# Performance work log

Measured on AMD Instinct MI355X. Metric: run time of the kernel, lower is better.

## Reference

```python
import jax, jax.numpy as jnp
import numpy as np

N_NODES = 100000
N_EDGES = 1600000
DIM = 128
N_LAYERS = 3
N_GRAPHS = 2048


def setup_inputs() -> dict:
    key = jax.random.key(0)
    ks = jax.random.split(key, 6)
    x = jax.random.normal(ks[0], (N_NODES, DIM), dtype=jnp.float32)
    edge_index = jax.random.randint(ks[1], (2, N_EDGES), 0, N_NODES, dtype=jnp.int64)
    batch = jnp.sort(jax.random.randint(ks[2], (N_NODES,), 0, N_GRAPHS, dtype=jnp.int64))
    scale = 1.0 / np.sqrt(DIM)
    W1 = jax.random.normal(ks[3], (N_LAYERS, DIM, DIM), dtype=jnp.float32) * scale
    b1 = jnp.zeros((N_LAYERS, DIM), dtype=jnp.float32)
    W2 = jax.random.normal(ks[4], (N_LAYERS, DIM, DIM), dtype=jnp.float32) * scale
    b2 = jnp.zeros((N_LAYERS, DIM), dtype=jnp.float32)
    return {"x": x, "edge_index": edge_index, "batch": batch,
            "W1": W1, "b1": b1, "W2": W2, "b2": b2}


def reference(x, edge_index, batch, W1, b1, W2, b2):
    src, dst = edge_index[0], edge_index[1]
    n = x.shape[0]
    n_layers = W1.shape[0]
    for l in range(n_layers):
        # GINConv (eps=0): h_i = MLP( sum_{j in N(i)} x_j + x_i )
        agg = jax.ops.segment_sum(x[src], dst, num_segments=n)  # [N, D]
        h = agg + x
        h = jnp.maximum(h @ W1[l] + b1[l], 0.0) @ W2[l] + b2[l]
        x = jnp.maximum(h, 0.0)  # outer self.act
    # global_mean_pool over graph ids
    sums = jax.ops.segment_sum(x, batch, num_segments=N_GRAPHS)  # [G, D]
    counts = jax.ops.segment_sum(jnp.ones((n,), x.dtype), batch, num_segments=N_GRAPHS)
    return sums / jnp.maximum(counts, 1.0)[:, None]
```

## Files before the change

kernel.cpp:

```cpp
#include <hip/hip_runtime.h>
#include <hip/hip_bf16.h>
#include <stdint.h>

#define N_NODES  100000
#define N_PAD    100032
#define N_EDGES  1600000
#define DIM      128
#define N_LAYERS 3
#define N_GRAPHS 2048

#define BSHIFT   9
#define NBUCKET  196
#define P1CHUNK  8192
#define P1GRID   196

typedef _Float16 f16;
typedef __attribute__((ext_vector_type(2))) _Float16 f16x2;
typedef __attribute__((ext_vector_type(8))) _Float16 f16x8;
typedef __attribute__((ext_vector_type(4))) float f32x4;

#define MFMA16(a, b, c) __builtin_amdgcn_mfma_f32_16x16x32_f16((a), (b), (c), 0, 0, 0)

#define OFF_OFFS  0u
#define OFF_BHT   400064u
#define OFF_BST   400896u
#define OFF_GCUR  401728u
#define OFF_BLKH  402560u
#define OFF_ESRC  556288u
#define OFF_PAIR  6956288u
#define OFF_X16   19756288u
#define OFF_A16   45364480u
#define OFF_B16   70972672u
#define OFF_W1T   96580864u
#define OFF_W2T   96679168u


__global__ __launch_bounds__(256) void k_bhist(const int* __restrict__ dst,
                                               int* __restrict__ btot, int* __restrict__ blkh) {
    __shared__ int h[NBUCKET];
    int tid = threadIdx.x, b = blockIdx.x;
    if (tid < NBUCKET) h[tid] = 0;
    __syncthreads();
    int base = b * P1CHUNK;
    int n = min(P1CHUNK, N_EDGES - base);
    for (int i = tid; i < n; i += 256)
        atomicAdd(&h[dst[base + i] >> BSHIFT], 1);
    __syncthreads();
    if (tid < NBUCKET) {
        blkh[b * NBUCKET + tid] = h[tid];
        atomicAdd(&btot[tid], h[tid]);
    }
}

__global__ void k_bscan(const int* __restrict__ btot, int* __restrict__ bstart,
                        int* __restrict__ gcursor, int* __restrict__ offs) {
    __shared__ int s[NBUCKET + 1];
    if (threadIdx.x == 0) {
        int run = 0;
        for (int i = 0; i < NBUCKET; i++) { s[i] = run; run += btot[i]; }
        s[NBUCKET] = run;
    }
    __syncthreads();
    int t = threadIdx.x;
    if (t <= NBUCKET) bstart[t] = s[t];
    if (t < NBUCKET)  gcursor[t] = s[t];
    if (t == 0) offs[N_NODES] = N_EDGES;
}

__global__ __launch_bounds__(256) void k_part1(const int* __restrict__ src, const int* __restrict__ dst,
                                               const int* __restrict__ blkh, int* __restrict__ gcursor,
                                               uint2* __restrict__ pairs) {
    __shared__ int gbase[NBUCKET];
    __shared__ int cur[NBUCKET];
    int tid = threadIdx.x, b = blockIdx.x;
    if (tid < NBUCKET) {
        int h = blkh[b * NBUCKET + tid];
        gbase[tid] = atomicAdd(&gcursor[tid], h);
        cur[tid] = 0;
    }
    __syncthreads();
    int base = b * P1CHUNK;
    int n = min(P1CHUNK, N_EDGES - base);
    for (int i = tid; i < n; i += 256) {
        int d = dst[base + i], s = src[base + i];
        int bin = d >> BSHIFT;
        int slot = atomicAdd(&cur[bin], 1);
        uint2 p; p.x = (unsigned)d; p.y = (unsigned)s;
        pairs[gbase[bin] + slot] = p;
    }
}

__global__ __launch_bounds__(256) void k_part2(const uint2* __restrict__ pairs,
                                               const int* __restrict__ bstart,
                                               int* __restrict__ offs, int* __restrict__ esrc) {
    __shared__ int cnt[512];
    __shared__ int excl[512];
    __shared__ int sc[256];
    int t = threadIdx.x, b = blockIdx.x;
    int n0 = b << BSHIFT;
    int nn = min(512, N_NODES - n0);
    int e0 = bstart[b], e1 = bstart[b + 1];
    cnt[t] = 0; cnt[t + 256] = 0;
    __syncthreads();
    for (int i = e0 + t; i < e1; i += 256)
        atomicAdd(&cnt[pairs[i].x & 511], 1);
    __syncthreads();
    int a = cnt[2 * t], psum = a + cnt[2 * t + 1];
    sc[t] = psum;
    __syncthreads();
    for (int off = 1; off < 256; off <<= 1) {
        int v = (t >= off) ? sc[t - off] : 0;
        __syncthreads();
        sc[t] += v;
        __syncthreads();
    }
    int pairExcl = sc[t] - psum;
    excl[2 * t] = pairExcl;
    excl[2 * t + 1] = pairExcl + a;
    __syncthreads();
    for (int j = t; j < nn; j += 256) offs[n0 + j] = e0 + excl[j];
    __syncthreads();
    for (int i = e0 + t; i < e1; i += 256) {
        uint2 p = pairs[i];
        int pos = e0 + atomicAdd(&excl[p.x & 511], 1);
        esrc[pos] = (int)p.y;
    }
}


__global__ void k_cvtX(const float* __restrict__ x, f16* __restrict__ o) {
    size_t i = ((size_t)blockIdx.x * 256 + threadIdx.x) * 8;
    float4 v0 = *(const float4*)&x[i];
    float4 v1 = *(const float4*)&x[i + 4];
    f16x8 h;
    h[0] = (f16)v0.x; h[1] = (f16)v0.y; h[2] = (f16)v0.z; h[3] = (f16)v0.w;
    h[4] = (f16)v1.x; h[5] = (f16)v1.y; h[6] = (f16)v1.z; h[7] = (f16)v1.w;
    *(f16x8*)&o[i] = h;
}

__global__ void k_cvtW(const float* __restrict__ W, f16* __restrict__ Wt) {
    int t = blockIdx.x * 256 + threadIdx.x;
    int l = t >> 14;
    int kn = t & 16383;
    int k = kn >> 7, n = kn & 127;
    Wt[l * 16384 + n * 128 + k] = (f16)W[t];
}


__global__ __launch_bounds__(256) void k_agg(const f16* __restrict__ x, const int* __restrict__ offs,
                                             const int* __restrict__ esrc, f16* __restrict__ out) {
    int tid = threadIdx.x;
    int node = blockIdx.x * 4 + (tid >> 6);
    int lane = tid & 63;
    int g = lane >> 4;
    int c = lane & 15;
    const f16x8* xr = (const f16x8*)x;
    int e0 = offs[node], e1 = offs[node + 1];

    float acc[8];
    f16x8 sv = xr[(size_t)node * 16 + c];
#pragma unroll
    for (int j = 0; j < 8; j++) acc[j] = (g == 0) ? (float)sv[j] : 0.f;

    int e = e0 + g;
    for (; e + 4 < e1; e += 8) {
        int s0 = esrc[e], s1 = esrc[e + 4];
        f16x8 v0 = xr[(size_t)s0 * 16 + c];
        f16x8 v1 = xr[(size_t)s1 * 16 + c];
#pragma unroll
        for (int j = 0; j < 8; j++) acc[j] += (float)v0[j] + (float)v1[j];
    }
    if (e < e1) {
        f16x8 v = xr[(size_t)esrc[e] * 16 + c];
#pragma unroll
        for (int j = 0; j < 8; j++) acc[j] += (float)v[j];
    }

#pragma unroll
    for (int j = 0; j < 8; j++) {
        acc[j] += __shfl_xor(acc[j], 16);
        acc[j] += __shfl_xor(acc[j], 32);
    }
    if (g == 0) {
        f16x8 o;
#pragma unroll
        for (int j = 0; j < 8; j++) o[j] = (f16)acc[j];
        ((f16x8*)out)[(size_t)node * 16 + c] = o;
    }
}


#define BM 64
#define LDS_K 136

__global__ __launch_bounds__(256) void k_mlp(const f16* __restrict__ in, f16* __restrict__ out,
                                             const f16* __restrict__ W1t, const float* __restrict__ b1,
                                             const f16* __restrict__ W2t, const float* __restrict__ b2) {
    __shared__ __align__(16) f16 tile[BM * LDS_K];
    int tid = threadIdx.x;
    int lane = tid & 63;
    int w = tid >> 6;
    int fr = lane & 15;
    int fg = lane >> 4;
    int row0 = blockIdx.x * BM;

    f16x8 w1f[2][4], w2f[2][4];
    float b1v[2], b2v[2];
#pragma unroll
    for (int nt = 0; nt < 2; nt++) {
        int col = w * 32 + nt * 16 + fr;
#pragma unroll
        for (int ks = 0; ks < 4; ks++) {
            int k = ks * 32 + fg * 8;
            w1f[nt][ks] = *(const f16x8*)&W1t[col * DIM + k];
            w2f[nt][ks] = *(const f16x8*)&W2t[col * DIM + k];
        }
        b1v[nt] = b1[col];
        b2v[nt] = b2[col];
    }

#pragma unroll
    for (int p = 0; p < 4; p++) {
        int idx = p * 256 + tid;
        int r = idx >> 4, c = idx & 15;
        *(float4*)&tile[r * LDS_K + c * 8] = *(const float4*)&in[(size_t)(row0 + r) * DIM + c * 8];
    }
    __syncthreads();

    f32x4 acc[4][2];
#pragma unroll
    for (int mt = 0; mt < 4; mt++)
#pragma unroll
        for (int nt = 0; nt < 2; nt++) acc[mt][nt] = (f32x4){0.f, 0.f, 0.f, 0.f};

#pragma unroll
    for (int mt = 0; mt < 4; mt++) {
#pragma unroll
        for (int ks = 0; ks < 4; ks++) {
            f16x8 a = *(const f16x8*)&tile[(mt * 16 + fr) * LDS_K + ks * 32 + fg * 8];
            acc[mt][0] = MFMA16(a, w1f[0][ks], acc[mt][0]);
            acc[mt][1] = MFMA16(a, w1f[1][ks], acc[mt][1]);
        }
    }
    __syncthreads();

#pragma unroll
    for (int mt = 0; mt < 4; mt++)
#pragma unroll
        for (int nt = 0; nt < 2; nt++) {
            int col = w * 32 + nt * 16 + fr;
#pragma unroll
            for (int r = 0; r < 4; r++) {
                int m = mt * 16 + fg * 4 + r;
                tile[m * LDS_K + col] = (f16)fmaxf(acc[mt][nt][r] + b1v[nt], 0.f);
            }
        }
    __syncthreads();

    f32x4 acc2[4][2];
#pragma unroll
    for (int mt = 0; mt < 4; mt++)
#pragma unroll
        for (int nt = 0; nt < 2; nt++) acc2[mt][nt] = (f32x4){0.f, 0.f, 0.f, 0.f};

#pragma unroll
    for (int mt = 0; mt < 4; mt++) {
#pragma unroll
        for (int ks = 0; ks < 4; ks++) {
            f16x8 a = *(const f16x8*)&tile[(mt * 16 + fr) * LDS_K + ks * 32 + fg * 8];
            acc2[mt][0] = MFMA16(a, w2f[0][ks], acc2[mt][0]);
            acc2[mt][1] = MFMA16(a, w2f[1][ks], acc2[mt][1]);
        }
    }
    __syncthreads();

#pragma unroll
    for (int mt = 0; mt < 4; mt++)
#pragma unroll
        for (int nt = 0; nt < 2; nt++) {
            int col = w * 32 + nt * 16 + fr;
#pragma unroll
            for (int r = 0; r < 4; r++) {
                int m = mt * 16 + fg * 4 + r;
                tile[m * LDS_K + col] = (f16)fmaxf(acc2[mt][nt][r] + b2v[nt], 0.f);
            }
        }
    __syncthreads();

#pragma unroll
    for (int p = 0; p < 4; p++) {
        int idx = p * 256 + tid;
        int r = idx >> 4, c = idx & 15;
        *(float4*)&out[(size_t)(row0 + r) * DIM + c * 8] = *(float4*)&tile[r * LDS_K + c * 8];
    }
}


__global__ void k_pool(const f16* __restrict__ xf, const int* __restrict__ batch,
                       float* __restrict__ out) {
    int g = blockIdx.x;
    int d = threadIdx.x;
    int lo = 0, hi = N_NODES;
    while (lo < hi) { int m = (lo + hi) >> 1; if (batch[m] < g) lo = m + 1; else hi = m; }
    int start = lo;
    hi = N_NODES;
    while (lo < hi) { int m = (lo + hi) >> 1; if (batch[m] <= g) lo = m + 1; else hi = m; }
    int end = lo;
    float acc = 0.f;
    for (int i = start; i < end; i++) acc += (float)xf[(size_t)i * DIM + d];
    float cntf = (float)(end - start);
    out[(size_t)g * DIM + d] = acc / fmaxf(cntf, 1.f);
}


extern "C" void kernel_launch(void* const* d_in, const int* in_sizes, int n_in,
                              void* d_out, int out_size, void* d_ws, size_t ws_size,
                              hipStream_t stream) {
    const float* x     = (const float*)d_in[0];
    const int*   ei    = (const int*)d_in[1];
    const int*   batch = (const int*)d_in[2];
    const float* W1    = (const float*)d_in[3];
    const float* b1    = (const float*)d_in[4];
    const float* W2    = (const float*)d_in[5];
    const float* b2    = (const float*)d_in[6];
    const int* src = ei;
    const int* dst = ei + N_EDGES;

    char* ws = (char*)d_ws;
    int*   offs  = (int*)(ws + OFF_OFFS);
    int*   btot  = (int*)(ws + OFF_BHT);
    int*   bst   = (int*)(ws + OFF_BST);
    int*   gcur  = (int*)(ws + OFF_GCUR);
    int*   blkh  = (int*)(ws + OFF_BLKH);
    int*   esrc  = (int*)(ws + OFF_ESRC);
    uint2* pairs = (uint2*)(ws + OFF_PAIR);
    f16*   x16   = (f16*)(ws + OFF_X16);
    f16*   a16   = (f16*)(ws + OFF_A16);
    f16*   b16   = (f16*)(ws + OFF_B16);
    f16*   w1t   = (f16*)(ws + OFF_W1T);
    f16*   w2t   = (f16*)(ws + OFF_W2T);
    float* outp  = (float*)d_out;

    hipMemsetAsync(btot, 0, NBUCKET * sizeof(int), stream);
    k_bhist<<<P1GRID, 256, 0, stream>>>(dst, btot, blkh);
    k_bscan<<<1, 256, 0, stream>>>(btot, bst, gcur, offs);
    k_part1<<<P1GRID, 256, 0, stream>>>(src, dst, blkh, gcur, pairs);
    k_part2<<<NBUCKET, 256, 0, stream>>>(pairs, bst, offs, esrc);

    k_cvtX<<<6250, 256, 0, stream>>>(x, x16);
    k_cvtW<<<192, 256, 0, stream>>>(W1, w1t);
    k_cvtW<<<192, 256, 0, stream>>>(W2, w2t);
    hipMemsetAsync(a16 + (size_t)N_NODES * DIM, 0, (size_t)(N_PAD - N_NODES) * DIM * sizeof(f16), stream);
    hipMemsetAsync(b16 + (size_t)N_NODES * DIM, 0, (size_t)(N_PAD - N_NODES) * DIM * sizeof(f16), stream);

    const f16* xin = x16;
    for (int l = 0; l < N_LAYERS; ++l) {
        f16* aggbuf = (l == 1) ? b16 : a16;
        k_agg<<<N_NODES / 4, 256, 0, stream>>>(xin, offs, esrc, aggbuf);
        k_mlp<<<N_PAD / BM, 256, 0, stream>>>(aggbuf, aggbuf,
                                              w1t + (size_t)l * DIM * DIM, b1 + (size_t)l * DIM,
                                              w2t + (size_t)l * DIM * DIM, b2 + (size_t)l * DIM);
        xin = aggbuf;
    }

    k_pool<<<N_GRAPHS, 128, 0, stream>>>(xin, batch, outp);
}
```

Baseline: 351.3 us.

## Fuse neighbor aggregation into MLP kernel with shuffle-broadcast edge indices

Merges the per-layer gather-sum aggregation into the MLP kernel: each block aggregates its 64 rows directly into LDS, then runs both matmuls. This removes a global write and read of the aggregated features and one launch per layer. Edge indices are loaded 16 at a time cooperatively and broadcast with shuffles, with four gathers in flight per iteration. The MFMA operands are swapped so each lane writes 4 contiguous output columns and can store them with vector writes straight to global memory. The risk is lower gather parallelism per block, since each wave now processes its nodes serially in groups of 4, and an occupancy hint of 4 blocks per CU.

```diff
diff --git a/kernel.cpp b/kernel.cpp
--- a/kernel.cpp
+++ b/kernel.cpp
@@ -16,6 +16,7 @@
 
 typedef _Float16 f16;
 typedef __attribute__((ext_vector_type(2))) _Float16 f16x2;
+typedef __attribute__((ext_vector_type(4))) _Float16 f16x4;
 typedef __attribute__((ext_vector_type(8))) _Float16 f16x8;
 typedef __attribute__((ext_vector_type(4))) float f32x4;
 
@@ -147,85 +148,83 @@
 }
 
 
-__global__ __launch_bounds__(256) void k_agg(const f16* __restrict__ x, const int* __restrict__ offs,
-                                             const int* __restrict__ esrc, f16* __restrict__ out) {
-    int tid = threadIdx.x;
-    int node = blockIdx.x * 4 + (tid >> 6);
-    int lane = tid & 63;
-    int g = lane >> 4;
-    int c = lane & 15;
-    const f16x8* xr = (const f16x8*)x;
-    int e0 = offs[node], e1 = offs[node + 1];
-
-    float acc[8];
-    f16x8 sv = xr[(size_t)node * 16 + c];
-#pragma unroll
-    for (int j = 0; j < 8; j++) acc[j] = (g == 0) ? (float)sv[j] : 0.f;
-
-    int e = e0 + g;
-    for (; e + 4 < e1; e += 8) {
-        int s0 = esrc[e], s1 = esrc[e + 4];
-        f16x8 v0 = xr[(size_t)s0 * 16 + c];
-        f16x8 v1 = xr[(size_t)s1 * 16 + c];
-#pragma unroll
-        for (int j = 0; j < 8; j++) acc[j] += (float)v0[j] + (float)v1[j];
-    }
-    if (e < e1) {
-        f16x8 v = xr[(size_t)esrc[e] * 16 + c];
-#pragma unroll
-        for (int j = 0; j < 8; j++) acc[j] += (float)v[j];
-    }
-
-#pragma unroll
-    for (int j = 0; j < 8; j++) {
-        acc[j] += __shfl_xor(acc[j], 16);
-        acc[j] += __shfl_xor(acc[j], 32);
-    }
-    if (g == 0) {
-        f16x8 o;
-#pragma unroll
-        for (int j = 0; j < 8; j++) o[j] = (f16)acc[j];
-        ((f16x8*)out)[(size_t)node * 16 + c] = o;
-    }
-}
-
-
 #define BM 64
 #define LDS_K 136
 
-__global__ __launch_bounds__(256) void k_mlp(const f16* __restrict__ in, f16* __restrict__ out,
-                                             const f16* __restrict__ W1t, const float* __restrict__ b1,
-                                             const f16* __restrict__ W2t, const float* __restrict__ b2) {
+__global__ __launch_bounds__(256, 4) void k_fused(
+    const f16* __restrict__ xin, f16* __restrict__ xout,
+    const int* __restrict__ offs, const int* __restrict__ esrc,
+    const f16* __restrict__ W1t, const float* __restrict__ b1,
+    const f16* __restrict__ W2t, const float* __restrict__ b2)
+{
     __shared__ __align__(16) f16 tile[BM * LDS_K];
-    int tid = threadIdx.x;
+    int tid  = threadIdx.x;
     int lane = tid & 63;
-    int w = tid >> 6;
-    int fr = lane & 15;
-    int fg = lane >> 4;
+    int w    = tid >> 6;
+    int fr   = lane & 15;
+    int fg   = lane >> 4;
     int row0 = blockIdx.x * BM;
 
-    f16x8 w1f[2][4], w2f[2][4];
-    float b1v[2], b2v[2];
+    {
+        int g = fg, c = fr;
+        const f16x8* xr = (const f16x8*)xin;
+        int srcLane = g << 4;
+#pragma unroll
+        for (int s_ = 0; s_ < 4; s_++) {
+            int node = row0 + w * 16 + s_ * 4 + g;
+            float acc[8];
+            if (node < N_NODES) {
+                int e0 = offs[node], e1 = offs[node + 1];
+                f16x8 sv = xr[(size_t)node * 16 + c];
+#pragma unroll
+                for (int j = 0; j < 8; j++) acc[j] = (float)sv[j];
+                for (int base = e0; base < e1; base += 16) {
+                    int ncur = e1 - base; if (ncur > 16) ncur = 16;
+                    int ev = esrc[base + (c < ncur ? c : ncur - 1)];
+                    int k = 0;
+                    for (; k + 4 <= ncur; k += 4) {
+                        int s0 = __shfl(ev, srcLane + k);
+                        int s1 = __shfl(ev, srcLane + k + 1);
+                        int s2 = __shfl(ev, srcLane + k + 2);
+                        int s3 = __shfl(ev, srcLane + k + 3);
+                        f16x8 v0 = xr[(size_t)s0 * 16 + c];
+                        f16x8 v1 = xr[(size_t)s1 * 16 + c];
+                        f16x8 v2 = xr[(size_t)s2 * 16 + c];
+                        f16x8 v3 = xr[(size_t)s3 * 16 + c];
+#pragma unroll
+                        for (int j = 0; j < 8; j++)
+                            acc[j] += (float)v0[j] + (float)v1[j] + (float)v2[j] + (float)v3[j];
+                    }
+                    for (; k < ncur; k++) {
+                        int s = __shfl(ev, srcLane + k);
+                        f16x8 v = xr[(size_t)s * 16 + c];
+#pragma unroll
+                        for (int j = 0; j < 8; j++) acc[j] += (float)v[j];
+                    }
+                }
+            } else {
+#pragma unroll
+                for (int j = 0; j < 8; j++) acc[j] = 0.f;
+            }
+            int r = w * 16 + s_ * 4 + g;
+            f16x8 o;
+#pragma unroll
+            for (int j = 0; j < 8; j++) o[j] = (f16)acc[j];
+            *(f16x8*)&tile[r * LDS_K + c * 8] = o;
+        }
+    }
+    __syncthreads();
+
+    f16x8 wf[2][4];
+    float4 bv[2];
 #pragma unroll
     for (int nt = 0; nt < 2; nt++) {
         int col = w * 32 + nt * 16 + fr;
 #pragma unroll
-        for (int ks = 0; ks < 4; ks++) {
-            int k = ks * 32 + fg * 8;
-            w1f[nt][ks] = *(const f16x8*)&W1t[col * DIM + k];
-            w2f[nt][ks] = *(const f16x8*)&W2t[col * DIM + k];
-        }
-        b1v[nt] = b1[col];
-        b2v[nt] = b2[col];
-    }
-
-#pragma unroll
-    for (int p = 0; p < 4; p++) {
-        int idx = p * 256 + tid;
-        int r = idx >> 4, c = idx & 15;
-        *(float4*)&tile[r * LDS_K + c * 8] = *(const float4*)&in[(size_t)(row0 + r) * DIM + c * 8];
-    }
-    __syncthreads();
+        for (int ks = 0; ks < 4; ks++)
+            wf[nt][ks] = *(const f16x8*)&W1t[col * DIM + ks * 32 + fg * 8];
+        bv[nt] = *(const float4*)&b1[w * 32 + nt * 16 + fg * 4];
+    }
 
     f32x4 acc[4][2];
 #pragma unroll
@@ -234,65 +233,62 @@
         for (int nt = 0; nt < 2; nt++) acc[mt][nt] = (f32x4){0.f, 0.f, 0.f, 0.f};
 
 #pragma unroll
-    for (int mt = 0; mt < 4; mt++) {
+    for (int mt = 0; mt < 4; mt++)
 #pragma unroll
         for (int ks = 0; ks < 4; ks++) {
             f16x8 a = *(const f16x8*)&tile[(mt * 16 + fr) * LDS_K + ks * 32 + fg * 8];
-            acc[mt][0] = MFMA16(a, w1f[0][ks], acc[mt][0]);
-            acc[mt][1] = MFMA16(a, w1f[1][ks], acc[mt][1]);
-        }
-    }
+            acc[mt][0] = MFMA16(wf[0][ks], a, acc[mt][0]);
+            acc[mt][1] = MFMA16(wf[1][ks], a, acc[mt][1]);
+        }
     __syncthreads();
 
 #pragma unroll
     for (int mt = 0; mt < 4; mt++)
 #pragma unroll
         for (int nt = 0; nt < 2; nt++) {
-            int col = w * 32 + nt * 16 + fr;
-#pragma unroll
-            for (int r = 0; r < 4; r++) {
-                int m = mt * 16 + fg * 4 + r;
-                tile[m * LDS_K + col] = (f16)fmaxf(acc[mt][nt][r] + b1v[nt], 0.f);
-            }
-        }
-    __syncthreads();
-
-    f32x4 acc2[4][2];
-#pragma unroll
-    for (int mt = 0; mt < 4; mt++)
-#pragma unroll
-        for (int nt = 0; nt < 2; nt++) acc2[mt][nt] = (f32x4){0.f, 0.f, 0.f, 0.f};
-
-#pragma unroll
-    for (int mt = 0; mt < 4; mt++) {
+            f16x4 hv;
+            hv[0] = (f16)fmaxf(acc[mt][nt][0] + bv[nt].x, 0.f);
+            hv[1] = (f16)fmaxf(acc[mt][nt][1] + bv[nt].y, 0.f);
+            hv[2] = (f16)fmaxf(acc[mt][nt][2] + bv[nt].z, 0.f);
+            hv[3] = (f16)fmaxf(acc[mt][nt][3] + bv[nt].w, 0.f);
+            *(f16x4*)&tile[(mt * 16 + fr) * LDS_K + w * 32 + nt * 16 + fg * 4] = hv;
+        }
+
+#pragma unroll
+    for (int nt = 0; nt < 2; nt++) {
+        int col = w * 32 + nt * 16 + fr;
+#pragma unroll
+        for (int ks = 0; ks < 4; ks++)
+            wf[nt][ks] = *(const f16x8*)&W2t[col * DIM + ks * 32 + fg * 8];
+        bv[nt] = *(const float4*)&b2[w * 32 + nt * 16 + fg * 4];
+    }
+    __syncthreads();
+
+#pragma unroll
+    for (int mt = 0; mt < 4; mt++)
+#pragma unroll
+        for (int nt = 0; nt < 2; nt++) acc[mt][nt] = (f32x4){0.f, 0.f, 0.f, 0.f};
+
+#pragma unroll
+    for (int mt = 0; mt < 4; mt++)
 #pragma unroll
         for (int ks = 0; ks < 4; ks++) {
             f16x8 a = *(const f16x8*)&tile[(mt * 16 + fr) * LDS_K + ks * 32 + fg * 8];
-            acc2[mt][0] = MFMA16(a, w2f[0][ks], acc2[mt][0]);
-            acc2[mt][1] = MFMA16(a, w2f[1][ks], acc2[mt][1]);
-        }
-    }
-    __syncthreads();
+            acc[mt][0] = MFMA16(wf[0][ks], a, acc[mt][0]);
+            acc[mt][1] = MFMA16(wf[1][ks], a, acc[mt][1]);
+        }
 
 #pragma unroll
     for (int mt = 0; mt < 4; mt++)
 #pragma unroll
         for (int nt = 0; nt < 2; nt++) {
-            int col = w * 32 + nt * 16 + fr;
-#pragma unroll
-            for (int r = 0; r < 4; r++) {
-                int m = mt * 16 + fg * 4 + r;
-                tile[m * LDS_K + col] = (f16)fmaxf(acc2[mt][nt][r] + b2v[nt], 0.f);
-            }
-        }
-    __syncthreads();
-
-#pragma unroll
-    for (int p = 0; p < 4; p++) {
-        int idx = p * 256 + tid;
-        int r = idx >> 4, c = idx & 15;
-        *(float4*)&out[(size_t)(row0 + r) * DIM + c * 8] = *(float4*)&tile[r * LDS_K + c * 8];
-    }
+            f16x4 ov;
+            ov[0] = (f16)fmaxf(acc[mt][nt][0] + bv[nt].x, 0.f);
+            ov[1] = (f16)fmaxf(acc[mt][nt][1] + bv[nt].y, 0.f);
+            ov[2] = (f16)fmaxf(acc[mt][nt][2] + bv[nt].z, 0.f);
+            ov[3] = (f16)fmaxf(acc[mt][nt][3] + bv[nt].w, 0.f);
+            *(f16x4*)&xout[(size_t)(row0 + mt * 16 + fr) * DIM + w * 32 + nt * 16 + fg * 4] = ov;
+        }
 }
 
 
@@ -350,17 +346,14 @@
     k_cvtX<<<6250, 256, 0, stream>>>(x, x16);
     k_cvtW<<<192, 256, 0, stream>>>(W1, w1t);
     k_cvtW<<<192, 256, 0, stream>>>(W2, w2t);
-    hipMemsetAsync(a16 + (size_t)N_NODES * DIM, 0, (size_t)(N_PAD - N_NODES) * DIM * sizeof(f16), stream);
-    hipMemsetAsync(b16 + (size_t)N_NODES * DIM, 0, (size_t)(N_PAD - N_NODES) * DIM * sizeof(f16), stream);
 
     const f16* xin = x16;
     for (int l = 0; l < N_LAYERS; ++l) {
-        f16* aggbuf = (l == 1) ? b16 : a16;
-        k_agg<<<N_NODES / 4, 256, 0, stream>>>(xin, offs, esrc, aggbuf);
-        k_mlp<<<N_PAD / BM, 256, 0, stream>>>(aggbuf, aggbuf,
-                                              w1t + (size_t)l * DIM * DIM, b1 + (size_t)l * DIM,
-                                              w2t + (size_t)l * DIM * DIM, b2 + (size_t)l * DIM);
-        xin = aggbuf;
+        f16* xoutb = (l == 1) ? b16 : a16;
+        k_fused<<<N_PAD / BM, 256, 0, stream>>>(xin, xoutb, offs, esrc,
+                                                w1t + (size_t)l * DIM * DIM, b1 + (size_t)l * DIM,
+                                                w2t + (size_t)l * DIM * DIM, b2 + (size_t)l * DIM);
+        xin = xoutb;
     }
 
     k_pool<<<N_GRAPHS, 128, 0, stream>>>(xin, batch, outp);
```

Result: no change. 349.8 us (-0.4%).
